# Optimization experiments

Measured on AMD Instinct MI355X. Metric: run time of the kernel, lower is better.

The kernel has to match this reference:

```python
import jax, jax.numpy as jnp
import numpy as np

B, S, D, U, E = 64, 512, 1024, 4096, 16


def setup_inputs() -> dict:
    key = jax.random.key(0)
    k1, k2, k3 = jax.random.split(key, 3)
    x = jax.random.normal(k1, (B, S, D), dtype=jnp.float32)
    index = jax.random.randint(k2, (B, 1), 0, E, dtype=jnp.int32)
    # glorot_uniform for (E, D, U) kernel
    limit = np.sqrt(6.0 / (D + U)).astype(np.float32)
    ws = jax.random.uniform(k3, (E, D, U), dtype=jnp.float32, minval=-limit, maxval=limit)
    bs = jnp.zeros((E, U), dtype=jnp.float32)
    return {"x": x, "ws": ws, "bs": bs, "index": index}


def reference(x, ws, bs, index):
    # tf.gather_nd(ws, index) with index shape (B, 1) == ws[index[:, 0]]
    idx = index[:, 0]                      # [B]
    w = ws[idx]                            # [B, D, U] per-group expert weights
    b = bs[idx]                            # [B, U]
    # einsum 'adb,abc->adc' in the original == bsd,bdu->bsu here
    out = jnp.einsum('bsd,bdu->bsu', x, w) + b[:, None, :]
    return jax.nn.relu(out)
```

## Files before the change

kernel.cpp:

```cpp
#include <hip/hip_runtime.h>


typedef float v4f  __attribute__((ext_vector_type(4)));
typedef _Float16 v8h __attribute__((ext_vector_type(8)));
typedef __fp16  v2fp __attribute__((ext_vector_type(2)));

constexpr int Bb = 64, Ss = 512, Dd = 1024, Uu = 4096, Ee = 16;
constexpr int BM = 128, BN = 128, BK = 32;
constexpr int KT = Dd / BK;
constexpr int BKP = 40;

typedef const __attribute__((address_space(1))) void gvoid_t;
typedef __attribute__((address_space(3))) void lvoid_t;
__device__ __forceinline__ void gl2lds16(const void* g, void* l) {
  __builtin_amdgcn_global_load_lds((gvoid_t*)g, (lvoid_t*)l, 16, 0, 0);
}

__global__ void perm_kernel(const int* __restrict__ index, int* __restrict__ perm,
                            int* __restrict__ used) {
  const int b = threadIdx.x;
  const int e = index[b];
  int pos = 0;
  for (int b2 = 0; b2 < Bb; ++b2) {
    const int e2 = index[b2];
    pos += (e2 < e) || (e2 == e && b2 < b);
  }
  perm[pos] = b;
  if (used != nullptr && b < Ee) {
    int u = 0;
    for (int b2 = 0; b2 < Bb; ++b2) u |= (index[b2] == b) ? 1 : 0;
    used[b] = u;
  }
}

__global__ __launch_bounds__(256) void convert_x(const float* __restrict__ in,
                                                 _Float16* __restrict__ outh) {
  const size_t i = ((size_t)blockIdx.x * 256 + threadIdx.x) * 8;
  const v4f a = *(const v4f*)(in + i);
  const v4f b = *(const v4f*)(in + i + 4);
  v8h h;
  #pragma unroll
  for (int j = 0; j < 4; ++j) h[j] = (_Float16)a[j];
  #pragma unroll
  for (int j = 0; j < 4; ++j) h[4 + j] = (_Float16)b[j];
  *(v8h*)(outh + i) = h;
}

__global__ __launch_bounds__(256) void transpose_w(const float* __restrict__ ws,
                                                   _Float16* __restrict__ wt,
                                                   const int* __restrict__ used) {
  const int e = blockIdx.z;
  if (!used[e]) return;
  const int u0 = blockIdx.x * 64;
  const int d0 = blockIdx.y * 64;
  __shared__ float tile[64][65];
  const int tid = threadIdx.x;
  {
    const int tu = (tid & 15) * 4;
    const int td = tid >> 4;
    const float* src = ws + (size_t)e * Dd * Uu + (size_t)d0 * Uu + u0;
    #pragma unroll
    for (int i = 0; i < 4; ++i) {
      const v4f v = *(const v4f*)(src + (size_t)(td + i * 16) * Uu + tu);
      tile[td + i * 16][tu + 0] = v[0];
      tile[td + i * 16][tu + 1] = v[1];
      tile[td + i * 16][tu + 2] = v[2];
      tile[td + i * 16][tu + 3] = v[3];
    }
  }
  __syncthreads();
  {
    const int tu = tid >> 2;
    const int tq = (tid & 3) * 16;
    _Float16* dst = wt + (size_t)e * Uu * Dd + (size_t)(u0 + tu) * Dd + d0 + tq;
    v8h h0, h1;
    #pragma unroll
    for (int j = 0; j < 8; ++j) h0[j] = (_Float16)tile[tq + j][tu];
    #pragma unroll
    for (int j = 0; j < 8; ++j) h1[j] = (_Float16)tile[tq + 8 + j][tu];
    *(v8h*)dst = h0;
    *(v8h*)(dst + 8) = h1;
  }
}

__global__ __launch_bounds__(256) void indexed_dense_gemm_h(
    const _Float16* __restrict__ xh, const _Float16* __restrict__ wt,
    const float* __restrict__ bs, const int* __restrict__ index,
    const int* __restrict__ perm, float* __restrict__ out) {
  const int bx = blockIdx.x;
  const int by = blockIdx.y;
  const int bz = perm[blockIdx.z];
  const int e  = index[bz];

  const int tid  = threadIdx.x;
  const int lane = tid & 63;
  const int wave = tid >> 6;

  const _Float16* A  = xh + (size_t)bz * (Ss * Dd) + (size_t)(by * BM) * Dd;
  const _Float16* Bt = wt + (size_t)e * (Dd * Uu) + (size_t)(bx * BN) * Dd;
  const float* bias  = bs + (size_t)e * Uu + bx * BN;
  float*       C     = out + (size_t)bz * (Ss * Uu) + (size_t)(by * BM) * Uu + bx * BN;

  __shared__ __align__(16) _Float16 As [2][BM * BK];
  __shared__ __align__(16) _Float16 Bsh[2][BN * BK];

  const int c0 = wave * 64;
  auto stage = [&](int buf, int kt) {
    const _Float16* a = A  + kt * BK;
    const _Float16* b = Bt + kt * BK;
    #pragma unroll
    for (int i = 0; i < 2; ++i) {
      const int cb  = c0 + i * 256;
      const int cl  = cb + lane;
      const int row = cl >> 2;
      const int kq  = (cl & 3) * 8;
      gl2lds16(a + (size_t)row * Dd + kq, &As [buf][cb * 8]);
      gl2lds16(b + (size_t)row * Dd + kq, &Bsh[buf][cb * 8]);
    }
  };

  const int fl = lane & 15;
  const int fq = lane >> 4;
  const int wm = (wave >> 1) * 64;
  const int wn = (wave & 1) * 64;
  const int aOff = (wm + fl) * BK + fq * 8;
  const int bOff = (wn + fl) * BK + fq * 8;

  v4f acc[4][4];
  #pragma unroll
  for (int i = 0; i < 4; ++i)
    #pragma unroll
    for (int j = 0; j < 4; ++j) acc[i][j] = {0.f, 0.f, 0.f, 0.f};

  stage(0, 0);
  __syncthreads();

  int buf = 0;
  for (int kt = 0; kt < KT; ++kt) {
    if (kt + 1 < KT) stage(buf ^ 1, kt + 1);

    v8h afr[4], bfr[4];
    #pragma unroll
    for (int mt = 0; mt < 4; ++mt) afr[mt] = *(const v8h*)&As [buf][aOff + mt * 16 * BK];
    #pragma unroll
    for (int nt = 0; nt < 4; ++nt) bfr[nt] = *(const v8h*)&Bsh[buf][bOff + nt * 16 * BK];

    #pragma unroll
    for (int mt = 0; mt < 4; ++mt)
      #pragma unroll
      for (int nt = 0; nt < 4; ++nt)
        acc[mt][nt] = __builtin_amdgcn_mfma_f32_16x16x32_f16(afr[mt], bfr[nt], acc[mt][nt], 0, 0, 0);

    if (kt + 1 < KT) {
      __syncthreads();
      buf ^= 1;
    }
  }

  float bv[4];
  #pragma unroll
  for (int nt = 0; nt < 4; ++nt) bv[nt] = bias[wn + nt * 16 + fl];

  const int row0 = wm + fq * 4;
  #pragma unroll
  for (int mt = 0; mt < 4; ++mt) {
    #pragma unroll
    for (int r = 0; r < 4; ++r) {
      float* crow = C + (size_t)(row0 + mt * 16 + r) * Uu + wn + fl;
      #pragma unroll
      for (int nt = 0; nt < 4; ++nt) {
        const float v = acc[mt][nt][r] + bv[nt];
        crow[nt * 16] = fmaxf(v, 0.0f);
      }
    }
  }
}

__global__ __launch_bounds__(256) void indexed_dense_gemm(
    const float* __restrict__ x, const float* __restrict__ ws,
    const float* __restrict__ bs, const int* __restrict__ index,
    const int* __restrict__ perm, float* __restrict__ out) {
  const int bx = blockIdx.x;
  const int by = blockIdx.y;
  const int bz = perm[blockIdx.z];
  const int e  = index[bz];

  const int tid  = threadIdx.x;
  const int lane = tid & 63;
  const int wave = tid >> 6;

  const float* A    = x   + (size_t)bz * (Ss * Dd) + (size_t)(by * BM) * Dd;
  const float* W    = ws  + (size_t)e * (Dd * Uu) + bx * BN;
  const float* bias = bs  + (size_t)e * Uu + bx * BN;
  float*       C    = out + (size_t)bz * (Ss * Uu) + (size_t)(by * BM) * Uu + bx * BN;

  __shared__ __align__(16) _Float16 As[BM * BKP];
  __shared__ __align__(16) _Float16 Bs[BN * BKP];

  const int am  = tid >> 1;
  const int ak0 = (tid & 1) * 16;
  const float* Aptr = A + am * Dd + ak0;
  _Float16* aWr = &As[am * BKP + ak0];

  const int bn  = (wave & 1) * 64 + lane;
  const int bk0 = (wave >> 1) * 16;
  const float* Wptr = W + (size_t)bk0 * Uu + bn;
  _Float16* bWr = &Bs[bn * BKP + bk0];

  const int fl = lane & 15;
  const int fq = lane >> 4;
  const int wm = (wave >> 1) * 64;
  const int wn = (wave & 1) * 64;
  const _Float16* aRd = &As[(wm + fl) * BKP + fq * 8];
  const _Float16* bRd = &Bs[(wn + fl) * BKP + fq * 8];

  v4f acc[4][4];
  #pragma unroll
  for (int i = 0; i < 4; ++i)
    #pragma unroll
    for (int j = 0; j < 4; ++j) acc[i][j] = {0.f, 0.f, 0.f, 0.f};

  v4f   aReg[4];
  float bReg[16];

  auto loadTile = [&](int kt) {
    const float* p = Aptr + kt * BK;
    #pragma unroll
    for (int i = 0; i < 4; ++i) aReg[i] = ((const v4f*)p)[i];
    const float* q = Wptr + (size_t)kt * (BK * Uu);
    #pragma unroll
    for (int j = 0; j < 16; ++j) bReg[j] = q[(size_t)j * Uu];
  };

  auto stage = [&]() {
    union { v8h v[2]; v2fp h[8]; } ua;
    const float* af = (const float*)aReg;
    #pragma unroll
    for (int i = 0; i < 8; ++i)
      ua.h[i] = __builtin_amdgcn_cvt_pkrtz(af[2 * i], af[2 * i + 1]);
    *(v8h*)(aWr)     = ua.v[0];
    *(v8h*)(aWr + 8) = ua.v[1];

    union { v8h v[2]; v2fp h[8]; } ub;
    #pragma unroll
    for (int i = 0; i < 8; ++i)
      ub.h[i] = __builtin_amdgcn_cvt_pkrtz(bReg[2 * i], bReg[2 * i + 1]);
    *(v8h*)(bWr)     = ub.v[0];
    *(v8h*)(bWr + 8) = ub.v[1];
  };

  loadTile(0);
  stage();
  __syncthreads();

  for (int kt = 0; kt < KT; ++kt) {
    if (kt + 1 < KT) loadTile(kt + 1);

    v8h afr[4], bfr[4];
    #pragma unroll
    for (int mt = 0; mt < 4; ++mt) afr[mt] = *(const v8h*)(aRd + mt * 16 * BKP);
    #pragma unroll
    for (int nt = 0; nt < 4; ++nt) bfr[nt] = *(const v8h*)(bRd + nt * 16 * BKP);

    #pragma unroll
    for (int mt = 0; mt < 4; ++mt)
      #pragma unroll
      for (int nt = 0; nt < 4; ++nt)
        acc[mt][nt] = __builtin_amdgcn_mfma_f32_16x16x32_f16(afr[mt], bfr[nt], acc[mt][nt], 0, 0, 0);

    __syncthreads();
    if (kt + 1 < KT) stage();
    __syncthreads();
  }

  float bv[4];
  #pragma unroll
  for (int nt = 0; nt < 4; ++nt) bv[nt] = bias[wn + nt * 16 + fl];

  const int row0 = wm + fq * 4;
  #pragma unroll
  for (int mt = 0; mt < 4; ++mt) {
    #pragma unroll
    for (int r = 0; r < 4; ++r) {
      float* crow = C + (size_t)(row0 + mt * 16 + r) * Uu + wn + fl;
      #pragma unroll
      for (int nt = 0; nt < 4; ++nt) {
        const float v = acc[mt][nt][r] + bv[nt];
        crow[nt * 16] = fmaxf(v, 0.0f);
      }
    }
  }
}

extern "C" void kernel_launch(void* const* d_in, const int* in_sizes, int n_in,
                              void* d_out, int out_size, void* d_ws, size_t ws_size,
                              hipStream_t stream) {
  const float* x    = (const float*)d_in[0];
  const float* wsP  = (const float*)d_in[1];
  const float* bsP  = (const float*)d_in[2];
  const int*   idx  = (const int*)d_in[3];
  float*       out  = (float*)d_out;

  const size_t szW  = (size_t)Ee * Dd * Uu * sizeof(_Float16);
  const size_t szX  = (size_t)Bb * Ss * Dd * sizeof(_Float16);
  const size_t need = szW + szX + 1024;

  if (ws_size >= need) {
    _Float16* wt  = (_Float16*)d_ws;
    _Float16* xh  = (_Float16*)((char*)d_ws + szW);
    int* perm = (int*)((char*)d_ws + szW + szX);
    int* used = perm + Bb;

    perm_kernel<<<1, 64, 0, stream>>>(idx, perm, used);
    convert_x<<<(Bb * Ss * Dd) / (256 * 8), 256, 0, stream>>>(x, xh);
    transpose_w<<<dim3(Uu / 64, Dd / 64, Ee), 256, 0, stream>>>(wsP, wt, used);

    dim3 grid(Uu / BN, Ss / BM, Bb);
    indexed_dense_gemm_h<<<grid, 256, 0, stream>>>(xh, wt, bsP, idx, perm, out);
  } else {
    int* perm = (int*)d_ws;
    perm_kernel<<<1, 64, 0, stream>>>(idx, perm, nullptr);
    dim3 grid(Uu / BN, Ss / BM, Bb);
    indexed_dense_gemm<<<grid, 256, 0, stream>>>(x, wsP, bsP, idx, perm, out);
  }
}
```

Measured before the change: 1.146 ms.

## Add 256x256-tile 8-wave fp16 GEMM with swizzled LDS and phased pipelining

Adds a new GEMM kernel with 256x256 output tiles, 512 threads, and 128KB of dynamic LDS. It uses XOR-swizzled LDS layouts, half-tile staging interleaved with MFMA phases, explicit barriers, vmcnt waits, and setprio around the MFMA blocks. The aim is more operand reuse per byte loaded and better overlap of global-to-LDS copies with matrix math. It falls back to the old kernel if the large-LDS attribute cannot be set. The cost is heavy register pressure and possibly lower occupancy.

After: 1.016 ms. 11.3% less time.

```diff
diff --git a/kernel.cpp b/kernel.cpp
--- a/kernel.cpp
+++ b/kernel.cpp
@@ -6,15 +6,16 @@
 typedef __fp16  v2fp __attribute__((ext_vector_type(2)));
 
 constexpr int Bb = 64, Ss = 512, Dd = 1024, Uu = 4096, Ee = 16;
-constexpr int BM = 128, BN = 128, BK = 32;
-constexpr int KT = Dd / BK;
-constexpr int BKP = 40;
 
 typedef const __attribute__((address_space(1))) void gvoid_t;
 typedef __attribute__((address_space(3))) void lvoid_t;
 __device__ __forceinline__ void gl2lds16(const void* g, void* l) {
   __builtin_amdgcn_global_load_lds((gvoid_t*)g, (lvoid_t*)l, 16, 0, 0);
 }
+
+#define BAR()  asm volatile("s_barrier" ::: "memory")
+#define LGK0() asm volatile("s_waitcnt lgkmcnt(0)" ::: "memory")
+#define VMW(n) asm volatile("s_waitcnt vmcnt(" #n ")" ::: "memory")
 
 __global__ void perm_kernel(const int* __restrict__ index, int* __restrict__ perm,
                             int* __restrict__ used) {
@@ -83,10 +84,148 @@
   }
 }
 
+__global__ __launch_bounds__(512, 2) void gemm_8p(
+    const _Float16* __restrict__ xh, const _Float16* __restrict__ wt,
+    const float* __restrict__ bs, const int* __restrict__ index,
+    const int* __restrict__ perm, float* __restrict__ out) {
+  extern __shared__ _Float16 lds[];
+  constexpr int A0 = 0, A1 = 16384, B0 = 32768, B1 = 49152;
+  constexpr int NIT = 8;
+
+  const int bx = blockIdx.x;
+  const int by = blockIdx.y;
+  const int bz = perm[blockIdx.z];
+  const int e  = index[bz];
+
+  const int tid  = threadIdx.x;
+  const int lane = tid & 63;
+  const int wave = tid >> 6;
+  const int wr = wave >> 2, wc = wave & 3;
+  const int fl = lane & 15, fq = lane >> 4;
+
+  const _Float16* Ag = xh + ((size_t)bz * Ss + by * 256) * Dd;
+  const _Float16* Bg = wt + ((size_t)e  * Uu + bx * 256) * Dd;
+  const float* bias  = bs + (size_t)e * Uu + bx * 256;
+  float* C = out + (size_t)bz * Ss * Uu + (size_t)(by * 256) * Uu + bx * 256;
+
+  auto stageHT = [&](int ldsBase, const _Float16* g, int half) {
+    #pragma unroll
+    for (int i = 0; i < 2; ++i) {
+      const int cb = i * 512 + wave * 64;
+      const int c  = cb + lane;
+      const int r  = half * 128 + (c >> 3);
+      const int sc = (c & 7) ^ (r & 7);
+      gl2lds16(g + (size_t)r * Dd + sc * 8, &lds[ldsBase + half * 8192 + cb * 8]);
+    }
+  };
+
+  const int aswz0 = ((0 + fq) ^ (fl & 7)) * 8;
+  const int aswz1 = ((4 + fq) ^ (fl & 7)) * 8;
+
+  v8h ar[4][2];
+  v8h br[4][2];
+  auto ldA = [&](int base, int mh) {
+    const int r0 = wr * 128 + mh * 64 + fl;
+    #pragma unroll
+    for (int mi = 0; mi < 4; ++mi) {
+      ar[mi][0] = *(const v8h*)&lds[base + (r0 + mi * 16) * 64 + aswz0];
+      ar[mi][1] = *(const v8h*)&lds[base + (r0 + mi * 16) * 64 + aswz1];
+    }
+  };
+  auto ldB = [&](int base, int nh) {
+    const int r0 = wc * 64 + nh * 32 + fl;
+    #pragma unroll
+    for (int nl = 0; nl < 2; ++nl) {
+      br[nh * 2 + nl][0] = *(const v8h*)&lds[base + (r0 + nl * 16) * 64 + aswz0];
+      br[nh * 2 + nl][1] = *(const v8h*)&lds[base + (r0 + nl * 16) * 64 + aswz1];
+    }
+  };
+
+  v4f acc[8][4];
+  #pragma unroll
+  for (int i = 0; i < 8; ++i)
+    #pragma unroll
+    for (int j = 0; j < 4; ++j) acc[i][j] = {0.f, 0.f, 0.f, 0.f};
+
+  auto mm = [&](int mh, int nh) {
+    __builtin_amdgcn_s_setprio(1);
+    #pragma unroll
+    for (int mi = 0; mi < 4; ++mi)
+      #pragma unroll
+      for (int nl = 0; nl < 2; ++nl) {
+        const int gi = mh * 4 + mi, ni = nh * 2 + nl;
+        acc[gi][ni] = __builtin_amdgcn_mfma_f32_16x16x32_f16(ar[mi][0], br[ni][0], acc[gi][ni], 0, 0, 0);
+        acc[gi][ni] = __builtin_amdgcn_mfma_f32_16x16x32_f16(ar[mi][1], br[ni][1], acc[gi][ni], 0, 0, 0);
+      }
+    __builtin_amdgcn_s_setprio(0);
+  };
+
+  stageHT(A0, Ag, 0); stageHT(A0, Ag, 1);
+  stageHT(B0, Bg, 0); stageHT(B0, Bg, 1);
+  stageHT(A1, Ag + 64, 0);
+  VMW(2); BAR();
+
+  for (int t = 0; t < NIT; ++t) {
+    const _Float16* Ao  = Ag + (2 * t + 1) * 64;
+    const _Float16* Bo  = Bg + (2 * t + 1) * 64;
+    const _Float16* Ae2 = Ag + (2 * t + 2) * 64;
+    const _Float16* Be2 = Bg + (2 * t + 2) * 64;
+    const _Float16* Ao3 = Ag + (2 * t + 3) * 64;
+    const bool st = (t < NIT - 1);
+
+    ldA(A0, 0); ldB(B0, 0);
+    stageHT(A1, Ao, 1);
+    BAR(); LGK0(); mm(0, 0); BAR();
+    ldB(B0, 1);
+    stageHT(B1, Bo, 0);
+    BAR(); LGK0(); mm(0, 1); BAR();
+    ldA(A0, 1);
+    stageHT(B1, Bo, 1);
+    BAR(); LGK0(); mm(1, 0); BAR();
+    if (st) stageHT(A0, Ae2, 0);
+    BAR(); LGK0(); mm(1, 1);
+    if (st) { VMW(2); } else { VMW(0); }
+    BAR();
+
+    ldA(A1, 0); ldB(B1, 0);
+    if (st) stageHT(A0, Ae2, 1);
+    BAR(); LGK0(); mm(0, 0); BAR();
+    ldB(B1, 1);
+    if (st) stageHT(B0, Be2, 0);
+    BAR(); LGK0(); mm(0, 1); BAR();
+    ldA(A1, 1);
+    if (st) stageHT(B0, Be2, 1);
+    BAR(); LGK0(); mm(1, 0); BAR();
+    if (st) stageHT(A1, Ao3, 0);
+    BAR(); LGK0(); mm(1, 1);
+    if (st) { VMW(2); }
+    BAR();
+  }
+
+  float bv[4];
+  #pragma unroll
+  for (int ni = 0; ni < 4; ++ni) bv[ni] = bias[wc * 64 + ni * 16 + fl];
+
+  #pragma unroll
+  for (int gi = 0; gi < 8; ++gi) {
+    #pragma unroll
+    for (int r = 0; r < 4; ++r) {
+      const int row = wr * 128 + gi * 16 + fq * 4 + r;
+      float* crow = C + (size_t)row * Uu + wc * 64 + fl;
+      #pragma unroll
+      for (int ni = 0; ni < 4; ++ni) {
+        const float v = acc[gi][ni][r] + bv[ni];
+        crow[ni * 16] = fmaxf(v, 0.0f);
+      }
+    }
+  }
+}
+
 __global__ __launch_bounds__(256) void indexed_dense_gemm_h(
     const _Float16* __restrict__ xh, const _Float16* __restrict__ wt,
     const float* __restrict__ bs, const int* __restrict__ index,
     const int* __restrict__ perm, float* __restrict__ out) {
+  constexpr int BM = 128, BN = 128, BK = 32, KT = Dd / BK;
   const int bx = blockIdx.x;
   const int by = blockIdx.y;
   const int bz = perm[blockIdx.z];
@@ -99,7 +238,7 @@
   const _Float16* A  = xh + (size_t)bz * (Ss * Dd) + (size_t)(by * BM) * Dd;
   const _Float16* Bt = wt + (size_t)e * (Dd * Uu) + (size_t)(bx * BN) * Dd;
   const float* bias  = bs + (size_t)e * Uu + bx * BN;
-  float*       C     = out + (size_t)bz * (Ss * Uu) + (size_t)(by * BM) * Uu + bx * BN;
+  float*       C     = out + (size_t)bz * Ss * Uu + (size_t)(by * BM) * Uu + bx * BN;
 
   __shared__ __align__(16) _Float16 As [2][BM * BK];
   __shared__ __align__(16) _Float16 Bsh[2][BN * BK];
@@ -180,6 +319,7 @@
     const float* __restrict__ x, const float* __restrict__ ws,
     const float* __restrict__ bs, const int* __restrict__ index,
     const int* __restrict__ perm, float* __restrict__ out) {
+  constexpr int BM = 128, BN = 128, BK = 32, KT = Dd / BK, BKP = 40;
   const int bx = blockIdx.x;
   const int by = blockIdx.y;
   const int bz = perm[blockIdx.z];
@@ -192,7 +332,7 @@
   const float* A    = x   + (size_t)bz * (Ss * Dd) + (size_t)(by * BM) * Dd;
   const float* W    = ws  + (size_t)e * (Dd * Uu) + bx * BN;
   const float* bias = bs  + (size_t)e * Uu + bx * BN;
-  float*       C    = out + (size_t)bz * (Ss * Uu) + (size_t)(by * BM) * Uu + bx * BN;
+  float*       C    = out + (size_t)bz * Ss * Uu + (size_t)(by * BM) * Uu + bx * BN;
 
   __shared__ __align__(16) _Float16 As[BM * BKP];
   __shared__ __align__(16) _Float16 Bs[BN * BKP];
@@ -305,6 +445,12 @@
   const size_t szX  = (size_t)Bb * Ss * Dd * sizeof(_Float16);
   const size_t need = szW + szX + 1024;
 
+  static bool bigLds = [] {
+    return hipFuncSetAttribute(reinterpret_cast<const void*>(gemm_8p),
+                               hipFuncAttributeMaxDynamicSharedMemorySize,
+                               131072) == hipSuccess;
+  }();
+
   if (ws_size >= need) {
     _Float16* wt  = (_Float16*)d_ws;
     _Float16* xh  = (_Float16*)((char*)d_ws + szW);
@@ -315,12 +461,17 @@
     convert_x<<<(Bb * Ss * Dd) / (256 * 8), 256, 0, stream>>>(x, xh);
     transpose_w<<<dim3(Uu / 64, Dd / 64, Ee), 256, 0, stream>>>(wsP, wt, used);
 
-    dim3 grid(Uu / BN, Ss / BM, Bb);
-    indexed_dense_gemm_h<<<grid, 256, 0, stream>>>(xh, wt, bsP, idx, perm, out);
+    if (bigLds) {
+      dim3 grid(Uu / 256, Ss / 256, Bb);
+      gemm_8p<<<grid, 512, 131072, stream>>>(xh, wt, bsP, idx, perm, out);
+    } else {
+      dim3 grid(Uu / 128, Ss / 128, Bb);
+      indexed_dense_gemm_h<<<grid, 256, 0, stream>>>(xh, wt, bsP, idx, perm, out);
+    }
   } else {
     int* perm = (int*)d_ws;
     perm_kernel<<<1, 64, 0, stream>>>(idx, perm, nullptr);
-    dim3 grid(Uu / BN, Ss / BM, Bb);
+    dim3 grid(Uu / 128, Ss / 128, Bb);
     indexed_dense_gemm<<<grid, 256, 0, stream>>>(x, wsP, bsP, idx, perm, out);
   }
 }
```
